# Kernel optimization log

Hardware: AMD Instinct MI355X
Metric: run time of the kernel (lower is better)

## Reference

```python
import jax, jax.numpy as jnp
import numpy as np

TEMPERATURE = 0.1

def setup_inputs() -> dict:
    key = jax.random.key(0)
    k1, k2 = jax.random.split(key)
    B, D, NUM_CLASSES = 4096, 512, 64
    emb = jax.random.normal(k1, (B, D), dtype=jnp.float32)
    # L2-normalize so sims/temperature stays in a safe range for exp()
    emb = emb / jnp.linalg.norm(emb, axis=1, keepdims=True)
    labels = jax.random.randint(k2, (B,), 0, NUM_CLASSES, dtype=jnp.int64)
    return {"embeddings": emb, "labels": labels}

def reference(embeddings, labels):
    B = embeddings.shape[0]
    # [B, B] similarity matrix, scaled by temperature
    sims = jnp.matmul(embeddings, embeddings.T) / TEMPERATURE
    same = labels[:, None] == labels[None, :]
    eye = jnp.eye(B, dtype=bool)
    pos_mask = (same & ~eye).astype(sims.dtype)   # positives, diagonal excluded
    neg_mask = (~same).astype(sims.dtype)          # negatives
    exp_s = jnp.exp(sims)
    # denominator[i] = sum over negatives of exp_s[i, :]
    denom = jnp.sum(exp_s * neg_mask, axis=1, keepdims=True)  # [B, 1]
    # per positive pair (i, j): -log(exp_s[i,j] / (denom[i] + exp_s[i,j]))
    per_pair = -jnp.log(exp_s / (denom + exp_s))
    loss_sum = jnp.sum(per_pair * pos_mask)
    num_pos = jnp.sum(pos_mask)
    return loss_sum / jnp.maximum(num_pos, 1.0)
```

## Files before the change

kernel.cpp:

```cpp
#include <hip/hip_runtime.h>
#include <hip/hip_bf16.h>

#define B_N 4096
#define D_K 512
#define INV_T 10.0f

#define BM 128
#define CPB 256
#define CS (B_N / CPB)
#define SLOTS 16


typedef __attribute__((ext_vector_type(8))) short short8;
typedef __attribute__((ext_vector_type(4))) float float4v;

static __device__ inline unsigned short f32_to_bf16_rne(float f) {
    unsigned int u = __float_as_uint(f);
    unsigned int lsb = (u >> 16) & 1u;
    u += 0x7fffu + lsb;
    return (unsigned short)(u >> 16);
}

__global__ __launch_bounds__(256) void k0_convert(const float* __restrict__ emb,
                                                  unsigned short* __restrict__ embT) {
    int tid = blockIdx.x * 256 + threadIdx.x;
    int row = tid >> 6;
    int kq  = tid & 63;
    const float* sp = emb + row * D_K + kq * 8;
    float4 v0 = *(const float4*)(sp);
    float4 v1 = *(const float4*)(sp + 4);
    ushort4 o0, o1;
    o0.x = f32_to_bf16_rne(v0.x); o0.y = f32_to_bf16_rne(v0.y);
    o0.z = f32_to_bf16_rne(v0.z); o0.w = f32_to_bf16_rne(v0.w);
    o1.x = f32_to_bf16_rne(v1.x); o1.y = f32_to_bf16_rne(v1.y);
    o1.z = f32_to_bf16_rne(v1.z); o1.w = f32_to_bf16_rne(v1.w);
    unsigned short* dp = embT + (((row >> 4) * 64 + kq) * 16 + (row & 15)) * 8;
    *(ushort4*)(dp)     = o0;
    *(ushort4*)(dp + 4) = o1;
}

__global__ __launch_bounds__(256, 2) void k1_denom(const unsigned short* __restrict__ embT,
                                                   const int* __restrict__ labels,
                                                   float* __restrict__ denomPart,
                                                   int* __restrict__ posCnt,
                                                   float* __restrict__ posS) {
    __shared__ float sPos[BM * SLOTS];
    __shared__ int   sCnt[BM];

    const int tid  = threadIdx.x;
    const int wave = tid >> 6;
    const int lane = tid & 63;
    const int quad = lane >> 4;
    const int l16  = lane & 15;
    const int bx   = blockIdx.x, by = blockIdx.y;

    const int rowBase = bx * BM;

    if (tid < BM) sCnt[tid] = 0;

    short8 afrag[2][16];
#pragma unroll
    for (int t = 0; t < 2; ++t) {
        const int g = bx * 8 + wave * 2 + t;
        const unsigned short* ap = embT + (g * 64 * 16 + lane) * 8;
#pragma unroll
        for (int kc = 0; kc < 16; ++kc)
            afrag[t][kc] = *(const short8*)(ap + kc * 4 * 16 * 8);
    }

    int labI[2][4];
#pragma unroll
    for (int t = 0; t < 2; ++t)
#pragma unroll
        for (int r = 0; r < 4; ++r)
            labI[t][r] = labels[rowBase + wave * 32 + t * 16 + quad * 4 + r];

    __syncthreads();

    float rowAcc[2][4] = {{0.f,0.f,0.f,0.f},{0.f,0.f,0.f,0.f}};

    for (int cg = 0; cg < CPB / 16; ++cg) {
        const int g2 = by * 16 + cg;
        const unsigned short* bp = embT + (g2 * 64 * 16 + lane) * 8;

        float4v acc[2];
        acc[0] = (float4v){0.f, 0.f, 0.f, 0.f};
        acc[1] = (float4v){0.f, 0.f, 0.f, 0.f};
#pragma unroll
        for (int kc = 0; kc < 16; ++kc) {
            short8 bfrag = *(const short8*)(bp + kc * 4 * 16 * 8);
            acc[0] = __builtin_amdgcn_mfma_f32_16x16x32_bf16(afrag[0][kc], bfrag, acc[0], 0, 0, 0);
            acc[1] = __builtin_amdgcn_mfma_f32_16x16x32_bf16(afrag[1][kc], bfrag, acc[1], 0, 0, 0);
        }

        const int col  = g2 * 16 + l16;
        const int labJ = labels[col];
#pragma unroll
        for (int t = 0; t < 2; ++t) {
#pragma unroll
            for (int r = 0; r < 4; ++r) {
                float s = acc[t][r] * INV_T;
                const int lr  = wave * 32 + t * 16 + quad * 4 + r;
                if (labJ != labI[t][r]) {
                    rowAcc[t][r] += __expf(s);
                } else if (col != rowBase + lr) {
                    int idx = atomicAdd(&sCnt[lr], 1);
                    if (idx < SLOTS) sPos[lr * SLOTS + idx] = s;
                }
            }
        }
    }

#pragma unroll
    for (int t = 0; t < 2; ++t)
#pragma unroll
        for (int r = 0; r < 4; ++r) {
            float v = rowAcc[t][r];
            v += __shfl_xor(v, 1);
            v += __shfl_xor(v, 2);
            v += __shfl_xor(v, 4);
            v += __shfl_xor(v, 8);
            if (l16 == 0)
                denomPart[(rowBase + wave * 32 + t * 16 + quad * 4 + r) * CS + by] = v;
        }

    __syncthreads();
    if (tid < BM) {
        const int row = rowBase + tid;
        const int c   = min(sCnt[tid], SLOTS);
        posCnt[row * CS + by] = c;
        for (int m = 0; m < c; ++m)
            posS[(row * CS + by) * SLOTS + m] = sPos[tid * SLOTS + m];
    }
}

__global__ __launch_bounds__(256) void k2_pos(const float* __restrict__ denomPart,
                                              const int* __restrict__ posCnt,
                                              const float* __restrict__ posS,
                                              float* __restrict__ termSum,
                                              float* __restrict__ cntF) {
    const int wave = threadIdx.x >> 6;
    const int lane = threadIdx.x & 63;
    const int i    = blockIdx.x * 4 + wave;

    float d = (lane < CS) ? denomPart[i * CS + lane] : 0.0f;
    float c = (lane < CS) ? (float)posCnt[i * CS + lane] : 0.0f;
#pragma unroll
    for (int off = 32; off; off >>= 1) {
        d += __shfl_xor(d, off);
        c += __shfl_xor(c, off);
    }

    float sum = 0.0f;
#pragma unroll
    for (int it = 0; it < (CS * SLOTS) / 64; ++it) {
        int slot = lane + it * 64;
        int b    = slot >> 4;
        int m    = slot & 15;
        int cb   = posCnt[i * CS + b];
        if (m < cb) {
            float s = posS[i * CS * SLOTS + slot];
            sum += __logf(d + __expf(s)) - s;
        }
    }
#pragma unroll
    for (int off = 32; off; off >>= 1) sum += __shfl_xor(sum, off);
    if (lane == 0) { termSum[i] = sum; cntF[i] = c; }
}

__global__ __launch_bounds__(256) void k3_final(const float* __restrict__ termSum,
                                                const float* __restrict__ cntF,
                                                float* __restrict__ out) {
    __shared__ float sL[256], sC[256];
    float ls = 0.0f, cs = 0.0f;
    for (int i = threadIdx.x; i < B_N; i += 256) { ls += termSum[i]; cs += cntF[i]; }
    sL[threadIdx.x] = ls; sC[threadIdx.x] = cs;
    __syncthreads();
    for (int s = 128; s; s >>= 1) {
        if (threadIdx.x < s) {
            sL[threadIdx.x] += sL[threadIdx.x + s];
            sC[threadIdx.x] += sC[threadIdx.x + s];
        }
        __syncthreads();
    }
    if (threadIdx.x == 0) out[0] = sL[0] / fmaxf(sC[0], 1.0f);
}

extern "C" void kernel_launch(void* const* d_in, const int* in_sizes, int n_in,
                              void* d_out, int out_size, void* d_ws, size_t ws_size,
                              hipStream_t stream) {
    const float* emb    = (const float*)d_in[0];
    const int*   labels = (const int*)d_in[1];
    float*       out    = (float*)d_out;

    char* ws = (char*)d_ws;
    float*          termSum   = (float*)(ws);
    float*          cntF      = (float*)(ws + 16384);
    float*          denomPart = (float*)(ws + 32768);
    int*            posCnt    = (int*)(ws + 294912);
    float*          posS      = (float*)(ws + 557056);
    unsigned short* embT      = (unsigned short*)(ws + 8388608);

    k0_convert<<<dim3(B_N * D_K / 8 / 256), dim3(256), 0, stream>>>(emb, embT);

    k1_denom<<<dim3(B_N / BM, CS), dim3(256), 0, stream>>>(embT, labels, denomPart, posCnt, posS);

    k2_pos<<<dim3(B_N / 4), dim3(256), 0, stream>>>(denomPart, posCnt, posS, termSum, cntF);

    k3_final<<<dim3(1), dim3(256), 0, stream>>>(termSum, cntF, out);
}
```

Before: 116.1 us.

## Stage shared B tiles in LDS with double-buffered global_load_lds, halve columns per block

Before, each of the four waves in a block loaded the same B-column fragments straight from global memory. Now each 16-column tile is loaded once per block into a double-buffered LDS array using direct global-to-LDS loads, prefetching the next tile while MFMAs run on the current one. Columns per block drop from 256 to 128, which doubles the grid and the number of partial denominator and positive slots. The per-column labels are preloaded into registers, and workspace offsets are enlarged to fit the bigger partial buffers. In exchange it adds a barrier per column tile, uses more LDS per block, and gives k2 twice as many partials to reduce.

```diff
diff --git a/kernel.cpp b/kernel.cpp
--- a/kernel.cpp
+++ b/kernel.cpp
@@ -6,8 +6,9 @@
 #define INV_T 10.0f
 
 #define BM 128
-#define CPB 256
+#define CPB 128
 #define CS (B_N / CPB)
+#define NCG (CPB / 16)
 #define SLOTS 16
 
 
@@ -44,6 +45,7 @@
                                                    float* __restrict__ denomPart,
                                                    int* __restrict__ posCnt,
                                                    float* __restrict__ posS) {
+    __shared__ unsigned short sB[2][16 * 512];
     __shared__ float sPos[BM * SLOTS];
     __shared__ int   sCnt[BM];
 
@@ -53,19 +55,33 @@
     const int quad = lane >> 4;
     const int l16  = lane & 15;
     const int bx   = blockIdx.x, by = blockIdx.y;
-
     const int rowBase = bx * BM;
 
     if (tid < BM) sCnt[tid] = 0;
+
+#define STAGE(buf, g2)                                                             \
+    {                                                                              \
+        _Pragma("unroll")                                                          \
+        for (int p = 0; p < 4; ++p) {                                              \
+            const int ch = (p * 4 + wave) * 64;                                    \
+            const unsigned short* gp = embT + ((g2) * 1024 + ch + lane) * 8;       \
+            __builtin_amdgcn_global_load_lds(                                      \
+                (const __attribute__((address_space(1))) unsigned int*)gp,         \
+                (__attribute__((address_space(3))) unsigned int*)(&sB[buf][ch * 8]),\
+                16, 0, 0);                                                         \
+        }                                                                          \
+    }
+
+    STAGE(0, by * NCG);
 
     short8 afrag[2][16];
 #pragma unroll
     for (int t = 0; t < 2; ++t) {
         const int g = bx * 8 + wave * 2 + t;
-        const unsigned short* ap = embT + (g * 64 * 16 + lane) * 8;
+        const unsigned short* ap = embT + (g * 1024 + lane) * 8;
 #pragma unroll
         for (int kc = 0; kc < 16; ++kc)
-            afrag[t][kc] = *(const short8*)(ap + kc * 4 * 16 * 8);
+            afrag[t][kc] = *(const short8*)(ap + kc * 64 * 8);
     }
 
     int labI[2][4];
@@ -75,33 +91,37 @@
         for (int r = 0; r < 4; ++r)
             labI[t][r] = labels[rowBase + wave * 32 + t * 16 + quad * 4 + r];
 
-    __syncthreads();
+    int labJ[NCG];
+#pragma unroll
+    for (int cg = 0; cg < NCG; ++cg)
+        labJ[cg] = labels[by * CPB + cg * 16 + l16];
 
     float rowAcc[2][4] = {{0.f,0.f,0.f,0.f},{0.f,0.f,0.f,0.f}};
 
-    for (int cg = 0; cg < CPB / 16; ++cg) {
-        const int g2 = by * 16 + cg;
-        const unsigned short* bp = embT + (g2 * 64 * 16 + lane) * 8;
-
+    for (int cg = 0; cg < NCG; ++cg) {
+        __syncthreads();
+        if (cg + 1 < NCG) STAGE((cg + 1) & 1, by * NCG + cg + 1);
+
+        const unsigned short* bt = sB[cg & 1];
         float4v acc[2];
         acc[0] = (float4v){0.f, 0.f, 0.f, 0.f};
         acc[1] = (float4v){0.f, 0.f, 0.f, 0.f};
 #pragma unroll
         for (int kc = 0; kc < 16; ++kc) {
-            short8 bfrag = *(const short8*)(bp + kc * 4 * 16 * 8);
+            short8 bfrag = *(const short8*)(bt + (((kc * 4 + quad) * 16) + l16) * 8);
             acc[0] = __builtin_amdgcn_mfma_f32_16x16x32_bf16(afrag[0][kc], bfrag, acc[0], 0, 0, 0);
             acc[1] = __builtin_amdgcn_mfma_f32_16x16x32_bf16(afrag[1][kc], bfrag, acc[1], 0, 0, 0);
         }
 
-        const int col  = g2 * 16 + l16;
-        const int labJ = labels[col];
+        const int col = by * CPB + cg * 16 + l16;
+        const int lJ  = labJ[cg];
 #pragma unroll
         for (int t = 0; t < 2; ++t) {
 #pragma unroll
             for (int r = 0; r < 4; ++r) {
                 float s = acc[t][r] * INV_T;
-                const int lr  = wave * 32 + t * 16 + quad * 4 + r;
-                if (labJ != labI[t][r]) {
+                const int lr = wave * 32 + t * 16 + quad * 4 + r;
+                if (lJ != labI[t][r]) {
                     rowAcc[t][r] += __expf(s);
                 } else if (col != rowBase + lr) {
                     int idx = atomicAdd(&sCnt[lr], 1);
@@ -132,6 +152,7 @@
         for (int m = 0; m < c; ++m)
             posS[(row * CS + by) * SLOTS + m] = sPos[tid * SLOTS + m];
     }
+#undef STAGE
 }
 
 __global__ __launch_bounds__(256) void k2_pos(const float* __restrict__ denomPart,
@@ -197,9 +218,9 @@
     float*          termSum   = (float*)(ws);
     float*          cntF      = (float*)(ws + 16384);
     float*          denomPart = (float*)(ws + 32768);
-    int*            posCnt    = (int*)(ws + 294912);
-    float*          posS      = (float*)(ws + 557056);
-    unsigned short* embT      = (unsigned short*)(ws + 8388608);
+    int*            posCnt    = (int*)(ws + 557056);
+    float*          posS      = (float*)(ws + 1081344);
+    unsigned short* embT      = (unsigned short*)(ws + 12582912);
 
     k0_convert<<<dim3(B_N * D_K / 8 / 256), dim3(256), 0, stream>>>(emb, embT);
 
```

Result: faster. 111.6 us (-3.9%).
